# Kernel tuning notes

Hardware: AMD Instinct MI355X
Metric: run time of the kernel (lower is better)

The kernel has to match this reference:

```python
import jax, jax.numpy as jnp
import numpy as np
import math

MODEL_DIM = 64
HEAD_DIM = 16


def setup_inputs() -> dict:
    key = jax.random.key(0)
    ks = jax.random.split(key, 9)
    B, T = 4, 4096
    idx = jax.random.normal(ks[0], (B, T, MODEL_DIM), dtype=jnp.float32)
    s_in = 1.0 / math.sqrt(MODEL_DIM)
    s_h = 1.0 / math.sqrt(HEAD_DIM)
    return {
        "idx": idx,
        "Wk": jax.random.normal(ks[1], (HEAD_DIM, MODEL_DIM), dtype=jnp.float32) * s_in,
        "bk": jax.random.normal(ks[2], (HEAD_DIM,), dtype=jnp.float32) * 0.02,
        "Wq": jax.random.normal(ks[3], (HEAD_DIM, MODEL_DIM), dtype=jnp.float32) * s_in,
        "bq": jax.random.normal(ks[4], (HEAD_DIM,), dtype=jnp.float32) * 0.02,
        "Wv": jax.random.normal(ks[5], (HEAD_DIM, MODEL_DIM), dtype=jnp.float32) * s_in,
        "bv": jax.random.normal(ks[6], (HEAD_DIM,), dtype=jnp.float32) * 0.02,
        "Wp": jax.random.normal(ks[7], (MODEL_DIM, HEAD_DIM), dtype=jnp.float32) * s_h,
        "bp": jax.random.normal(ks[8], (MODEL_DIM,), dtype=jnp.float32) * 0.02,
    }


def reference(idx, Wk, bk, Wq, bq, Wv, bv, Wp, bp):
    # idx: [B, T, model_dim]
    k = idx @ Wk.T + bk  # [B, T, H]
    q = idx @ Wq.T + bq
    v = idx @ Wv.T + bv
    scale = 1.0 / math.sqrt(HEAD_DIM)
    att = jnp.einsum("bth,bsh->bts", q, k) * scale  # [B, T, T]
    att = jnp.tril(att)
    # faithful to masked_fill(attention == 0, -inf): any exact-zero entry
    # (upper triangle after tril, plus accidental zeros) becomes -inf
    att = jnp.where(att == 0, -jnp.inf, att)
    att = jax.nn.softmax(att, axis=-1)
    av = jnp.einsum("bts,bsh->bth", att, v)  # [B, T, H]
    return av @ Wp.T + bp  # [B, T, model_dim]
```

## Files before the change

### kernel.cpp

```cpp
#include <hip/hip_runtime.h>
#include <hip/hip_bf16.h>
#include <stdint.h>

#define DEV __device__ __forceinline__

typedef short s4v __attribute__((ext_vector_type(4)));
typedef float f4v __attribute__((ext_vector_type(4)));

static constexpr int T = 4096;
static constexpr int BATCH = 4;
static constexpr int MD = 64;
static constexpr int H = 16;
static constexpr int PB = T * H;

#if __has_builtin(__builtin_amdgcn_mfma_f32_16x16x16bf16_1k)
DEV f4v mfma16(s4v a, s4v b, f4v c) {
    return __builtin_amdgcn_mfma_f32_16x16x16bf16_1k(a, b, c, 0, 0, 0);
}
#elif __has_builtin(__builtin_amdgcn_mfma_f32_16x16x16_bf16)
typedef __bf16 bf4v __attribute__((ext_vector_type(4)));
DEV f4v mfma16(s4v a, s4v b, f4v c) {
    return __builtin_amdgcn_mfma_f32_16x16x16_bf16(__builtin_bit_cast(bf4v, a),
                                                   __builtin_bit_cast(bf4v, b), c, 0, 0, 0);
}
#else
DEV f4v mfma16(s4v a, s4v b, f4v c) {
    asm("v_mfma_f32_16x16x16_bf16 %0, %1, %2, %0" : "+v"(c) : "v"(a), "v"(b));
    return c;
}
#endif

DEV short f2bf(float x) {
    uint32_t u = __builtin_bit_cast(uint32_t, x);
    u += 0x7fffu + ((u >> 16) & 1u);
    return (short)(u >> 16);
}

DEV s4v pack4(f4v p) {
    return s4v{f2bf(p.x), f2bf(p.y), f2bf(p.z), f2bf(p.w)};
}

DEV float ex2(float x) {
#if __has_builtin(__builtin_amdgcn_exp2f)
    return __builtin_amdgcn_exp2f(x);
#else
    return exp2f(x);
#endif
}

__global__ __launch_bounds__(256) void k_proj(
    const float* __restrict__ idx,
    const float* __restrict__ Wk, const float* __restrict__ bk,
    const float* __restrict__ Wq, const float* __restrict__ bq,
    const float* __restrict__ Wv, const float* __restrict__ bv,
    short* __restrict__ qp, short* __restrict__ kp, short* __restrict__ vp)
{
    const int w = threadIdx.x >> 6, lane = threadIdx.x & 63;
    const int a = lane & 15, g = lane >> 4;
    const int tile = blockIdx.x * 4 + w;
    const int b = tile >> 8;
    const int trow0 = (tile & 255) << 4;

    const float* rb = idx + (size_t)(b * T + trow0) * MD;

    s4v xf[4], wqf[4], wkf[4], wvf[4];
#pragma unroll
    for (int kc = 0; kc < 4; ++kc) {
        const int ko = kc * 16 + 4 * g;
        f4v x = *(const f4v*)(rb + a * MD + ko);
        f4v q = *(const f4v*)(Wq + a * MD + ko);
        f4v k = *(const f4v*)(Wk + a * MD + ko);
        f4v v = *(const f4v*)(Wv + a * MD + ko);
        xf[kc]  = pack4(x);
        wqf[kc] = pack4(q);
        wkf[kc] = pack4(k);
        wvf[kc] = pack4(v);
    }
    f4v aq = {0.f,0.f,0.f,0.f}, ak = {0.f,0.f,0.f,0.f}, av = {0.f,0.f,0.f,0.f};
#pragma unroll
    for (int kc = 0; kc < 4; ++kc) {
        aq = mfma16(wqf[kc], xf[kc], aq);
        ak = mfma16(wkf[kc], xf[kc], ak);
        av = mfma16(xf[kc], wvf[kc], av);
    }
    const int slot = b * PB + (tile & 255) * 256 + g * 64 + a * 4;
    f4v bqv = *(const f4v*)(bq + 4 * g);
    f4v bkv = *(const f4v*)(bk + 4 * g);
    const float bvs = bv[a];
    const float CS = 0.36067376022224085f;
    f4v qv = {(aq.x + bqv.x) * CS, (aq.y + bqv.y) * CS,
              (aq.z + bqv.z) * CS, (aq.w + bqv.w) * CS};
    f4v kv = {ak.x + bkv.x, ak.y + bkv.y, ak.z + bkv.z, ak.w + bkv.w};
    f4v vv = {av.x + bvs, av.y + bvs, av.z + bvs, av.w + bvs};
    *(s4v*)(qp + slot) = pack4(qv);
    *(s4v*)(kp + slot) = pack4(kv);
    *(s4v*)(vp + slot) = pack4(vv);
}

DEV void proc_range(int lo, int hi, s4v Qf, int tq, int g,
                    const short* __restrict__ kb, const short* __restrict__ vb,
                    f4v& acc, float& lp)
{
    if (lo >= hi) return;
    const int ng = (hi - lo + 7) >> 3;
    s4v KA[8], VA[8], KB[8], VB[8];

    auto LOADG = [&](s4v* K, s4v* V, int gi) {
        const int st = lo + gi * 8;
#pragma unroll
        for (int u = 0; u < 8; ++u) {
            const int idx = min(st + u, hi - 1);
            K[u] = *(const s4v*)(kb + idx * 256);
            V[u] = *(const s4v*)(vb + idx * 256);
        }
    };
    auto COMPG = [&](const s4v* K, const s4v* V, int gi) {
        const int st = lo + gi * 8;
        if (gi == ng - 1) {
#pragma unroll
            for (int u = 0; u < 8; ++u) {
                if (st + u < hi) {
                    f4v S = mfma16(K[u], Qf, f4v{0.f,0.f,0.f,0.f});
                    const int sb = (st + u) * 16 + 4 * g;
                    f4v p;
#pragma unroll
                    for (int r = 0; r < 4; ++r) {
                        const float e = ex2(S[r]);
                        p[r] = (sb + r <= tq) ? e : 0.f;
                    }
                    lp += p.x + p.y + p.z + p.w;
                    acc = mfma16(pack4(p), V[u], acc);
                }
            }
        } else {
#pragma unroll
            for (int u = 0; u < 8; ++u) {
                f4v S = mfma16(K[u], Qf, f4v{0.f,0.f,0.f,0.f});
                f4v p;
#pragma unroll
                for (int r = 0; r < 4; ++r) p[r] = ex2(S[r]);
                lp += p.x + p.y + p.z + p.w;
                acc = mfma16(pack4(p), V[u], acc);
            }
        }
    };

    int it = 0;
    LOADG(KA, VA, 0);
    for (; it + 2 <= ng; it += 2) {
        LOADG(KB, VB, it + 1);
        COMPG(KA, VA, it);
        if (it + 2 < ng) LOADG(KA, VA, it + 2);
        COMPG(KB, VB, it + 1);
    }
    if (it < ng) COMPG(KA, VA, it);
}

__global__ __launch_bounds__(512, 4) void k_fused(
    const short* __restrict__ qp, const short* __restrict__ kp,
    const short* __restrict__ vp,
    const float* __restrict__ Wp, const float* __restrict__ bp,
    float* __restrict__ out)
{
    const int bx = blockIdx.x;
    const int b = bx >> 7, j = bx & 127;
    const int tid = threadIdx.x;
    const int w = tid >> 6, lane = tid & 63;
    const int a = lane & 15, g = lane >> 4;

    const int qtA = j, qtB = 255 - j;
    const int ntA = j + 1;
    const int ntot = 257;

    const short* qb = qp + b * PB;
    const short* kb = kp + b * PB + g * 64 + a * 4;
    const short* vb = vp + b * PB + g * 64 + a * 4;

    const s4v QfA = *(const s4v*)(qb + qtA * 256 + g * 64 + a * 4);
    const s4v QfB = *(const s4v*)(qb + qtB * 256 + g * 64 + a * 4);
    const int tqA = qtA * 16 + a, tqB = qtB * 16 + a;

    const int vLo = (ntot * w) >> 3;
    const int vHi = (ntot * (w + 1)) >> 3;

    f4v accA = {0.f,0.f,0.f,0.f}, accB = {0.f,0.f,0.f,0.f};
    float lpA = 0.f, lpB = 0.f;

    proc_range(vLo, min(vHi, ntA), QfA, tqA, g, kb, vb, accA, lpA);
    proc_range(max(vLo - ntA, 0), vHi - ntA, QfB, tqB, g, kb, vb, accB, lpB);

    __shared__ float pacc[16 * 64 * 4];
    __shared__ float plp[16 * 16];

    *(f4v*)&pacc[((w * 2 + 0) * 64 + lane) * 4] = accA;
    *(f4v*)&pacc[((w * 2 + 1) * 64 + lane) * 4] = accB;

    float lA = lpA + __shfl_xor(lpA, 16); lA += __shfl_xor(lA, 32);
    float lB = lpB + __shfl_xor(lpB, 16); lB += __shfl_xor(lB, 32);
    if (lane < 16) {
        plp[(w * 2 + 0) * 16 + lane] = lA;
        plp[(w * 2 + 1) * 16 + lane] = lB;
    }
    __syncthreads();

    if (tid < 128) {
        const int X = tid >> 6, i = (tid >> 2) & 15, dc = tid & 3;
        float av[16];
#pragma unroll
        for (int h = 0; h < 16; ++h) av[h] = 0.f;
        float l = 0.f;
#pragma unroll
        for (int ww = 0; ww < 8; ++ww) {
            const int base = ((ww * 2 + X) * 64 + (i >> 2) * 16) * 4 + (i & 3);
#pragma unroll
            for (int h = 0; h < 16; ++h) av[h] += pacc[base + h * 4];
            l += plp[(ww * 2 + X) * 16 + i];
        }
        const float inv = 1.f / l;
        const int qt = X ? qtB : qtA;

        float* orow = out + ((size_t)(b * T) + qt * 16 + i) * 64 + dc * 16;
#pragma unroll
        for (int j4 = 0; j4 < 4; ++j4) {
            f4v o;
#pragma unroll
            for (int jj = 0; jj < 4; ++jj) {
                const int d = dc * 16 + j4 * 4 + jj;
                const float* wr = Wp + d * 16;
                float s = 0.f;
#pragma unroll
                for (int h = 0; h < 16; ++h) s += av[h] * wr[h];
                o[jj] = bp[d] + s * inv;
            }
            *(f4v*)(orow + j4 * 4) = o;
        }
    }
}

extern "C" void kernel_launch(void* const* d_in, const int* in_sizes, int n_in,
                              void* d_out, int out_size, void* d_ws, size_t ws_size,
                              hipStream_t stream) {
    const float* idx = (const float*)d_in[0];
    const float* Wk  = (const float*)d_in[1];
    const float* bk  = (const float*)d_in[2];
    const float* Wq  = (const float*)d_in[3];
    const float* bq  = (const float*)d_in[4];
    const float* Wv  = (const float*)d_in[5];
    const float* bv  = (const float*)d_in[6];
    const float* Wp  = (const float*)d_in[7];
    const float* bp  = (const float*)d_in[8];
    float* out = (float*)d_out;

    short* qp = (short*)d_ws;
    short* kp = qp + BATCH * PB;
    short* vp = kp + BATCH * PB;

    k_proj<<<256, 256, 0, stream>>>(idx, Wk, bk, Wq, bq, Wv, bv, qp, kp, vp);
    k_fused<<<512, 512, 0, stream>>>(qp, kp, vp, Wp, bp, out);
}
```

Measured before the change: 29.83 us.

## Share K/V tile loads between paired query tiles and peel diagonal masking

The attention loop now processes the two paired query tiles (j and 255-j) together over their shared key range, so each K/V fragment loaded from memory feeds both tiles' MFMAs. The work split across the 8 waves is recomputed so that dual-query tiles count double. The causal mask check moves out of the hot loop into a separate diagonal-tile helper. This cuts global K/V load traffic and mask branching, at the cost of more register pressure in the dual path and more complex range bookkeeping.

```diff
diff --git a/kernel.cpp b/kernel.cpp
--- a/kernel.cpp
+++ b/kernel.cpp
@@ -97,9 +97,10 @@
     *(s4v*)(vp + slot) = pack4(vv);
 }
 
-DEV void proc_range(int lo, int hi, s4v Qf, int tq, int g,
-                    const short* __restrict__ kb, const short* __restrict__ vb,
-                    f4v& acc, float& lp)
+template<bool DUAL>
+DEV void run_fast(int lo, int hi, s4v QfA, s4v QfB,
+                  const short* __restrict__ kb, const short* __restrict__ vb,
+                  f4v& accA, float& lpA, f4v& accB, float& lpB)
 {
     if (lo >= hi) return;
     const int ng = (hi - lo + 7) >> 3;
@@ -114,34 +115,31 @@
             V[u] = *(const s4v*)(vb + idx * 256);
         }
     };
+    auto BODY = [&](s4v K, s4v V) {
+        if constexpr (DUAL) {
+            f4v SA = mfma16(K, QfA, f4v{0.f,0.f,0.f,0.f});
+            f4v pa;
+#pragma unroll
+            for (int r = 0; r < 4; ++r) pa[r] = ex2(SA[r]);
+            lpA += pa.x + pa.y + pa.z + pa.w;
+            accA = mfma16(pack4(pa), V, accA);
+        }
+        f4v SB = mfma16(K, QfB, f4v{0.f,0.f,0.f,0.f});
+        f4v pb;
+#pragma unroll
+        for (int r = 0; r < 4; ++r) pb[r] = ex2(SB[r]);
+        lpB += pb.x + pb.y + pb.z + pb.w;
+        accB = mfma16(pack4(pb), V, accB);
+    };
     auto COMPG = [&](const s4v* K, const s4v* V, int gi) {
         const int st = lo + gi * 8;
         if (gi == ng - 1) {
 #pragma unroll
-            for (int u = 0; u < 8; ++u) {
-                if (st + u < hi) {
-                    f4v S = mfma16(K[u], Qf, f4v{0.f,0.f,0.f,0.f});
-                    const int sb = (st + u) * 16 + 4 * g;
-                    f4v p;
-#pragma unroll
-                    for (int r = 0; r < 4; ++r) {
-                        const float e = ex2(S[r]);
-                        p[r] = (sb + r <= tq) ? e : 0.f;
-                    }
-                    lp += p.x + p.y + p.z + p.w;
-                    acc = mfma16(pack4(p), V[u], acc);
-                }
-            }
+            for (int u = 0; u < 8; ++u)
+                if (st + u < hi) BODY(K[u], V[u]);
         } else {
 #pragma unroll
-            for (int u = 0; u < 8; ++u) {
-                f4v S = mfma16(K[u], Qf, f4v{0.f,0.f,0.f,0.f});
-                f4v p;
-#pragma unroll
-                for (int r = 0; r < 4; ++r) p[r] = ex2(S[r]);
-                lp += p.x + p.y + p.z + p.w;
-                acc = mfma16(pack4(p), V[u], acc);
-            }
+            for (int u = 0; u < 8; ++u) BODY(K[u], V[u]);
         }
     };
 
@@ -156,6 +154,35 @@
     if (it < ng) COMPG(KA, VA, it);
 }
 
+DEV void tile_masked(int st, int g, s4v Qf1, int tq1,
+                     const short* __restrict__ kb, const short* __restrict__ vb,
+                     f4v& acc1, float& lp1,
+                     bool dual, s4v Qf2, f4v& acc2, float& lp2)
+{
+    const s4v K = *(const s4v*)(kb + st * 256);
+    const s4v V = *(const s4v*)(vb + st * 256);
+    const int sb = st * 16 + 4 * g;
+    {
+        f4v S = mfma16(K, Qf1, f4v{0.f,0.f,0.f,0.f});
+        f4v p;
+#pragma unroll
+        for (int r = 0; r < 4; ++r) {
+            const float e = ex2(S[r]);
+            p[r] = (sb + r <= tq1) ? e : 0.f;
+        }
+        lp1 += p.x + p.y + p.z + p.w;
+        acc1 = mfma16(pack4(p), V, acc1);
+    }
+    if (dual) {
+        f4v S = mfma16(K, Qf2, f4v{0.f,0.f,0.f,0.f});
+        f4v p;
+#pragma unroll
+        for (int r = 0; r < 4; ++r) p[r] = ex2(S[r]);
+        lp2 += p.x + p.y + p.z + p.w;
+        acc2 = mfma16(pack4(p), V, acc2);
+    }
+}
+
 __global__ __launch_bounds__(512, 4) void k_fused(
     const short* __restrict__ qp, const short* __restrict__ kp,
     const short* __restrict__ vp,
@@ -170,7 +197,7 @@
 
     const int qtA = j, qtB = 255 - j;
     const int ntA = j + 1;
-    const int ntot = 257;
+    const int NP  = 256 - j;
 
     const short* qb = qp + b * PB;
     const short* kb = kp + b * PB + g * 64 + a * 4;
@@ -180,14 +207,26 @@
     const s4v QfB = *(const s4v*)(qb + qtB * 256 + g * 64 + a * 4);
     const int tqA = qtA * 16 + a, tqB = qtB * 16 + a;
 
-    const int vLo = (ntot * w) >> 3;
-    const int vHi = (ntot * (w + 1)) >> 3;
+    auto cut = [&](int ww) -> int {
+        const int c = (257 * ww) >> 3;
+        return (c < 2 * ntA) ? ((c + 1) >> 1) : (c - ntA);
+    };
+    const int t0 = cut(w), t1 = cut(w + 1);
 
     f4v accA = {0.f,0.f,0.f,0.f}, accB = {0.f,0.f,0.f,0.f};
     float lpA = 0.f, lpB = 0.f;
 
-    proc_range(vLo, min(vHi, ntA), QfA, tqA, g, kb, vb, accA, lpA);
-    proc_range(max(vLo - ntA, 0), vHi - ntA, QfB, tqB, g, kb, vb, accB, lpB);
+    const int dEnd = min(t1, ntA);
+    run_fast<true>(t0, min(dEnd, j), QfA, QfB, kb, vb, accA, lpA, accB, lpB);
+    if (dEnd == ntA && t0 <= j)
+        tile_masked(j, g, QfA, tqA, kb, vb, accA, lpA, true, QfB, accB, lpB);
+
+    const int bLo = max(t0, ntA);
+    run_fast<false>(bLo, (t1 == NP) ? (NP - 1) : t1,
+                    QfA, QfB, kb, vb, accA, lpA, accB, lpB);
+    if (t1 == NP && bLo <= NP - 1)
+        tile_masked(NP - 1, g, QfB, tqB, kb, vb, accB, lpB,
+                    false, QfB, accB, lpB);
 
     __shared__ float pacc[16 * 64 * 4];
     __shared__ float plp[16 * 16];
```

Result: slower. 32.71 us (+9.7%).
